# Kernel tuning notes

Hardware: AMD Instinct MI355X
Metric: run time of the kernel (lower is better)

## Reference

```python
import jax, jax.numpy as jnp
import numpy as np

DIM = 128
BATCH = 1024


def _init_linear(key, fan_in, fan_out):
    kw, kb = jax.random.split(key)
    bound = 1.0 / np.sqrt(fan_in)
    W = jax.random.uniform(kw, (fan_in, fan_out), jnp.float32, -bound, bound)
    b = jax.random.uniform(kb, (fan_out,), jnp.float32, -bound, bound)
    return W, b


def setup_inputs() -> dict:
    key = jax.random.key(0)
    kx, ky, k1, k2, k3, k4 = jax.random.split(key, 6)
    x = jax.random.normal(kx, (BATCH, DIM), jnp.float32)
    y = jax.random.normal(ky, (BATCH, DIM), jnp.float32)
    W1, b1 = _init_linear(k1, 2 * DIM, 128)
    W2, b2 = _init_linear(k2, 128, 64)
    W3, b3 = _init_linear(k3, 64, 8)
    W4, b4 = _init_linear(k4, 8, 1)
    return {"x": x, "y": y, "W1": W1, "b1": b1, "W2": W2, "b2": b2,
            "W3": W3, "b3": b3, "W4": W4, "b4": b4}


def reference(x, y, W1, b1, W2, b2, W3, b3, W4, b4):
    # Original: pairs[i, j] = concat(x[j], y[i]); scores -> [B, B]; return transpose,
    # i.e. out[a, b] = f(concat(x[a], y[b])).
    # Split first linear algebraically: concat(x, y) @ W1 = x @ W1[:d] + y @ W1[d:].
    d = x.shape[1]
    xa = x @ W1[:d]          # [B, 128]
    yb = y @ W1[d:]          # [B, 128]
    h = jax.nn.relu(xa[:, None, :] + yb[None, :, :] + b1)  # [B, B, 128]
    h = jax.nn.relu(h @ W2 + b2)                            # [B, B, 64]
    h = jax.nn.relu(h @ W3 + b3)                            # [B, B, 8]
    out = (h @ W4 + b4)[..., 0]                             # [B, B]
    return out
```

## Files before the change

kernel.cpp:

```cpp
#include <hip/hip_runtime.h>
#include <hip/hip_bf16.h>

typedef float f32x4 __attribute__((ext_vector_type(4)));
typedef float f32x16 __attribute__((ext_vector_type(16)));
typedef short s16x8 __attribute__((ext_vector_type(8)));
typedef unsigned int u32x4 __attribute__((ext_vector_type(4)));

#define YB_PITCH 132

__device__ __forceinline__ short f2bf(float v) {
    __hip_bfloat16 h = __float2bfloat16(v);
    return __builtin_bit_cast(short, h);
}
__device__ __forceinline__ unsigned cvtpk(float lo, float hi) {
    unsigned r;
    asm("v_cvt_pk_bf16_f32 %0, %1, %2" : "=v"(r) : "v"(lo), "v"(hi));
    return r;
}
__device__ __forceinline__ void swap32(unsigned &x, unsigned &y) {
    asm("v_permlane32_swap_b32 %0, %1" : "+v"(x), "+v"(y));
}

__global__ __launch_bounds__(128) void precompute_kernel(
    const float* __restrict__ x, const float* __restrict__ y,
    const float* __restrict__ W1, const float* __restrict__ b1,
    float* __restrict__ xa, float* __restrict__ yb)
{
    __shared__ float rows[8][128];
    const int bid = blockIdx.x;
    const int k = threadIdx.x;
    const bool is_x = bid < 128;
    const int r0 = (is_x ? bid : bid - 128) * 8;
    const float* src = (is_x ? x : y) + (size_t)r0 * 128;
    const float* w = is_x ? W1 : (W1 + 128 * 128);
#pragma unroll
    for (int r = 0; r < 8; ++r) rows[r][k] = src[r * 128 + k];
    __syncthreads();
    float acc[8];
    const float bias = is_x ? b1[k] : 0.0f;
#pragma unroll
    for (int r = 0; r < 8; ++r) acc[r] = bias;
    for (int d = 0; d < 128; ++d) {
        float wv = w[d * 128 + k];
#pragma unroll
        for (int r = 0; r < 8; ++r) acc[r] = fmaf(rows[r][d], wv, acc[r]);
    }
    float* dst = (is_x ? xa : yb) + (size_t)r0 * 128 + k;
#pragma unroll
    for (int r = 0; r < 8; ++r) dst[r * 128] = acc[r];
}

__global__ __launch_bounds__(256, 2) void fused_kernel(
    const float* __restrict__ xa, const float* __restrict__ yb,
    const float* __restrict__ W2, const float* __restrict__ b2,
    const float* __restrict__ W3, const float* __restrict__ b3,
    const float* __restrict__ W4, const float* __restrict__ b4,
    float* __restrict__ out)
{
    __shared__ float yb_lds[128 * YB_PITCH];
    __shared__ float xa_lds[16 * 128];

    const int tid = threadIdx.x;
    const int bid = blockIdx.x;
    const int a_chunk = bid >> 3;
    const int bquad = bid & 7;
    const int wave = tid >> 6;
    const int lane = tid & 63;
    const int half = lane >> 5;
    const int m = lane & 31;

    {
        const f32x4* ysrc = (const f32x4*)(yb + (size_t)bquad * 128 * 128);
        for (int i = tid; i < 128 * 32; i += 256) {
            int row = i >> 5, c4 = i & 31;
            *(f32x4*)&yb_lds[row * YB_PITCH + c4 * 4] = ysrc[i];
        }
        const f32x4* xsrc = (const f32x4*)(xa + (size_t)a_chunk * 16 * 128);
        for (int i = tid; i < 16 * 32; i += 256) {
            int row = i >> 5, c4 = i & 31;
            *(f32x4*)&xa_lds[row * 128 + c4 * 4] = xsrc[i];
        }
    }

    s16x8 W2a[2][8];
#pragma unroll
    for (int mt = 0; mt < 2; ++mt)
#pragma unroll
        for (int s = 0; s < 8; ++s)
#pragma unroll
            for (int j = 0; j < 8; ++j)
                W2a[mt][s][j] = f2bf(W2[(s * 16 + half * 8 + j) * 64 + mt * 32 + m]);

    s16x8 W3a[4];
#pragma unroll
    for (int s = 0; s < 4; ++s)
#pragma unroll
        for (int j = 0; j < 8; ++j)
            W3a[s][j] = (m < 8) ? f2bf(W3[(s * 16 + half * 8 + j) * 8 + m]) : (short)0;

    f32x16 b2v0, b2v1;
#pragma unroll
    for (int r = 0; r < 16; ++r) {
        int f = (r & 3) + 8 * (r >> 2) + 4 * half;
        b2v0[r] = b2[f];
        b2v1[r] = b2[f + 32];
    }
    float b3v[4], w4v[4];
#pragma unroll
    for (int j = 0; j < 4; ++j) {
        b3v[j] = b3[j + 4 * half];
        w4v[j] = W4[j + 4 * half];
    }
    const float b4s = b4[0];

    __syncthreads();

    const float* ybrow = &yb_lds[(wave * 32 + m) * YB_PITCH + half * 8];
    const int bg = bquad * 4 + wave;

    for (int ai = 0; ai < 16; ++ai) {
        const float* xr = &xa_lds[ai * 128 + half * 8];
        f32x16 c20 = b2v0, c21 = b2v1;
#pragma unroll
        for (int s = 0; s < 8; ++s) {
            f32x4 x0 = *(const f32x4*)&xr[s * 16];
            f32x4 x1 = *(const f32x4*)&xr[s * 16 + 4];
            f32x4 y0 = *(const f32x4*)&ybrow[s * 16];
            f32x4 y1 = *(const f32x4*)&ybrow[s * 16 + 4];
            f32x4 h0 = x0 + y0, h1 = x1 + y1;
            u32x4 q;
            q.x = cvtpk(fmaxf(h0.x, 0.f), fmaxf(h0.y, 0.f));
            q.y = cvtpk(fmaxf(h0.z, 0.f), fmaxf(h0.w, 0.f));
            q.z = cvtpk(fmaxf(h1.x, 0.f), fmaxf(h1.y, 0.f));
            q.w = cvtpk(fmaxf(h1.z, 0.f), fmaxf(h1.w, 0.f));
            s16x8 bfrag = __builtin_bit_cast(s16x8, q);
            c20 = __builtin_amdgcn_mfma_f32_32x32x16_bf16(W2a[0][s], bfrag, c20, 0, 0, 0);
            c21 = __builtin_amdgcn_mfma_f32_32x32x16_bf16(W2a[1][s], bfrag, c21, 0, 0, 0);
        }

        unsigned P[8], Q[8];
#pragma unroll
        for (int i = 0; i < 8; ++i) {
            P[i] = cvtpk(fmaxf(c20[2 * i], 0.f), fmaxf(c20[2 * i + 1], 0.f));
            Q[i] = cvtpk(fmaxf(c21[2 * i], 0.f), fmaxf(c21[2 * i + 1], 0.f));
        }
        s16x8 bf3[4];
        {
            unsigned w0 = P[0], w2 = P[2]; swap32(w0, w2);
            unsigned w1 = P[1], w3 = P[3]; swap32(w1, w3);
            u32x4 t; t.x = w0; t.y = w1; t.z = w2; t.w = w3;
            bf3[0] = __builtin_bit_cast(s16x8, t);
            unsigned v0 = P[4], v2 = P[6]; swap32(v0, v2);
            unsigned v1 = P[5], v3 = P[7]; swap32(v1, v3);
            u32x4 u; u.x = v0; u.y = v1; u.z = v2; u.w = v3;
            bf3[1] = __builtin_bit_cast(s16x8, u);
            unsigned a0 = Q[0], a2 = Q[2]; swap32(a0, a2);
            unsigned a1 = Q[1], a3 = Q[3]; swap32(a1, a3);
            u32x4 t2; t2.x = a0; t2.y = a1; t2.z = a2; t2.w = a3;
            bf3[2] = __builtin_bit_cast(s16x8, t2);
            unsigned e0 = Q[4], e2 = Q[6]; swap32(e0, e2);
            unsigned e1 = Q[5], e3 = Q[7]; swap32(e1, e3);
            u32x4 u2; u2.x = e0; u2.y = e1; u2.z = e2; u2.w = e3;
            bf3[3] = __builtin_bit_cast(s16x8, u2);
        }

        f32x16 c3 = {};
        c3[0] = b3v[0]; c3[1] = b3v[1]; c3[2] = b3v[2]; c3[3] = b3v[3];
#pragma unroll
        for (int s = 0; s < 4; ++s)
            c3 = __builtin_amdgcn_mfma_f32_32x32x16_bf16(W3a[s], bf3[s], c3, 0, 0, 0);

        float p = fmaxf(c3[0], 0.f) * w4v[0] + fmaxf(c3[1], 0.f) * w4v[1]
                + fmaxf(c3[2], 0.f) * w4v[2] + fmaxf(c3[3], 0.f) * w4v[3];
        unsigned pu = __builtin_bit_cast(unsigned, p);
        unsigned pv = pu;
        asm("" : "+v"(pv));
        swap32(pu, pv);
        float r = __builtin_bit_cast(float, pu) + __builtin_bit_cast(float, pv) + b4s;
        if (half == 0)
            out[(size_t)(a_chunk * 16 + ai) * 1024 + bg * 32 + m] = r;
    }
}

extern "C" void kernel_launch(void* const* d_in, const int* in_sizes, int n_in,
                              void* d_out, int out_size, void* d_ws, size_t ws_size,
                              hipStream_t stream) {
    const float* x  = (const float*)d_in[0];
    const float* y  = (const float*)d_in[1];
    const float* W1 = (const float*)d_in[2];
    const float* b1 = (const float*)d_in[3];
    const float* W2 = (const float*)d_in[4];
    const float* b2 = (const float*)d_in[5];
    const float* W3 = (const float*)d_in[6];
    const float* b3 = (const float*)d_in[7];
    const float* W4 = (const float*)d_in[8];
    const float* b4 = (const float*)d_in[9];
    float* out = (float*)d_out;

    float* xa = (float*)d_ws;
    float* yb = xa + 1024 * 128;

    precompute_kernel<<<dim3(256), dim3(128), 0, stream>>>(x, y, W1, b1, xa, yb);
    fused_kernel<<<dim3(512), dim3(256), 0, stream>>>(xa, yb, W2, b2, W3, b3, W4, b4, out);
}
```

Measured before the change: 44.36 us.

## Form the layer-1 broadcast add with an MFMA and keep yb in registers

Drops the large yb LDS tile and instead holds each wave's yb rows in registers as MFMA accumulators. For each x row it computes xa+yb with an MFMA against a ones-vector B fragment, with xa as the A operand and Y as the C input. The result is then relu'd, packed to bf16 and lane-swapped into the B-fragment layout for the layer-2 MFMA. This removes the per-iteration LDS reads of yb and the vector adds, and frees a lot of LDS for occupancy. In exchange it adds extra MFMAs, permlane swaps and register pressure, and xa is now rounded to bf16 before the add, which changes accuracy.

```diff
diff --git a/kernel.cpp b/kernel.cpp
--- a/kernel.cpp
+++ b/kernel.cpp
@@ -5,8 +5,6 @@
 typedef float f32x16 __attribute__((ext_vector_type(16)));
 typedef short s16x8 __attribute__((ext_vector_type(8)));
 typedef unsigned int u32x4 __attribute__((ext_vector_type(4)));
-
-#define YB_PITCH 132
 
 __device__ __forceinline__ short f2bf(float v) {
     __hip_bfloat16 h = __float2bfloat16(v);
@@ -57,29 +55,35 @@
     const float* __restrict__ W4, const float* __restrict__ b4,
     float* __restrict__ out)
 {
-    __shared__ float yb_lds[128 * YB_PITCH];
     __shared__ float xa_lds[16 * 128];
 
     const int tid = threadIdx.x;
     const int bid = blockIdx.x;
     const int a_chunk = bid >> 3;
-    const int bquad = bid & 7;
+    const int bq = bid & 7;
     const int wave = tid >> 6;
     const int lane = tid & 63;
     const int half = lane >> 5;
     const int m = lane & 31;
+    const int bg = bq * 4 + wave;
 
     {
-        const f32x4* ysrc = (const f32x4*)(yb + (size_t)bquad * 128 * 128);
-        for (int i = tid; i < 128 * 32; i += 256) {
-            int row = i >> 5, c4 = i & 31;
-            *(f32x4*)&yb_lds[row * YB_PITCH + c4 * 4] = ysrc[i];
-        }
         const f32x4* xsrc = (const f32x4*)(xa + (size_t)a_chunk * 16 * 128);
-        for (int i = tid; i < 16 * 32; i += 256) {
-            int row = i >> 5, c4 = i & 31;
-            *(f32x4*)&xa_lds[row * 128 + c4 * 4] = xsrc[i];
-        }
+        f32x4* dst = (f32x4*)xa_lds;
+        for (int i = tid; i < 16 * 32; i += 256) dst[i] = xsrc[i];
+    }
+
+    f32x16 Y[4];
+    {
+        const float* yrow = yb + (size_t)(bg * 32 + m) * 128 + half * 4;
+#pragma unroll
+        for (int t = 0; t < 4; ++t)
+#pragma unroll
+            for (int g = 0; g < 4; ++g) {
+                f32x4 v = *(const f32x4*)&yrow[t * 32 + g * 8];
+                Y[t][4 * g + 0] = v.x; Y[t][4 * g + 1] = v.y;
+                Y[t][4 * g + 2] = v.z; Y[t][4 * g + 3] = v.w;
+            }
     }
 
     s16x8 W2a[2][8];
@@ -97,6 +101,10 @@
 #pragma unroll
         for (int j = 0; j < 8; ++j)
             W3a[s][j] = (m < 8) ? f2bf(W3[(s * 16 + half * 8 + j) * 8 + m]) : (short)0;
+
+    u32x4 ow = {0u, 0u, 0u, 0u};
+    ow.x = (half == 0) ? 0x00003F80u : 0u;
+    const s16x8 ones = __builtin_bit_cast(s16x8, ow);
 
     f32x16 b2v0, b2v1;
 #pragma unroll
@@ -115,27 +123,37 @@
 
     __syncthreads();
 
-    const float* ybrow = &yb_lds[(wave * 32 + m) * YB_PITCH + half * 8];
-    const int bg = bquad * 4 + wave;
+    float* outp = out + (size_t)(a_chunk * 16) * 1024 + bg * 32 + m;
 
     for (int ai = 0; ai < 16; ++ai) {
-        const float* xr = &xa_lds[ai * 128 + half * 8];
         f32x16 c20 = b2v0, c21 = b2v1;
-#pragma unroll
-        for (int s = 0; s < 8; ++s) {
-            f32x4 x0 = *(const f32x4*)&xr[s * 16];
-            f32x4 x1 = *(const f32x4*)&xr[s * 16 + 4];
-            f32x4 y0 = *(const f32x4*)&ybrow[s * 16];
-            f32x4 y1 = *(const f32x4*)&ybrow[s * 16 + 4];
-            f32x4 h0 = x0 + y0, h1 = x1 + y1;
-            u32x4 q;
-            q.x = cvtpk(fmaxf(h0.x, 0.f), fmaxf(h0.y, 0.f));
-            q.y = cvtpk(fmaxf(h0.z, 0.f), fmaxf(h0.w, 0.f));
-            q.z = cvtpk(fmaxf(h1.x, 0.f), fmaxf(h1.y, 0.f));
-            q.w = cvtpk(fmaxf(h1.z, 0.f), fmaxf(h1.w, 0.f));
-            s16x8 bfrag = __builtin_bit_cast(s16x8, q);
-            c20 = __builtin_amdgcn_mfma_f32_32x32x16_bf16(W2a[0][s], bfrag, c20, 0, 0, 0);
-            c21 = __builtin_amdgcn_mfma_f32_32x32x16_bf16(W2a[1][s], bfrag, c21, 0, 0, 0);
+
+#pragma unroll
+        for (int t = 0; t < 4; ++t) {
+            float xv = xa_lds[ai * 128 + t * 32 + m];
+            unsigned pk = cvtpk(xv, xv);
+            u32x4 aw; aw.x = pk; aw.y = pk; aw.z = pk; aw.w = pk;
+            s16x8 af = __builtin_bit_cast(s16x8, aw);
+            f32x16 S = __builtin_amdgcn_mfma_f32_32x32x16_bf16(af, ones, Y[t], 0, 0, 0);
+
+            unsigned P[8];
+#pragma unroll
+            for (int i = 0; i < 8; ++i)
+                P[i] = cvtpk(fmaxf(S[2 * i], 0.f), fmaxf(S[2 * i + 1], 0.f));
+
+            unsigned w0 = P[0], w2 = P[2]; swap32(w0, w2);
+            unsigned w1 = P[1], w3 = P[3]; swap32(w1, w3);
+            u32x4 q0; q0.x = w0; q0.y = w1; q0.z = w2; q0.w = w3;
+            s16x8 bf0 = __builtin_bit_cast(s16x8, q0);
+            unsigned v0 = P[4], v2 = P[6]; swap32(v0, v2);
+            unsigned v1 = P[5], v3 = P[7]; swap32(v1, v3);
+            u32x4 q1; q1.x = v0; q1.y = v1; q1.z = v2; q1.w = v3;
+            s16x8 bf1 = __builtin_bit_cast(s16x8, q1);
+
+            c20 = __builtin_amdgcn_mfma_f32_32x32x16_bf16(W2a[0][2 * t], bf0, c20, 0, 0, 0);
+            c21 = __builtin_amdgcn_mfma_f32_32x32x16_bf16(W2a[1][2 * t], bf0, c21, 0, 0, 0);
+            c20 = __builtin_amdgcn_mfma_f32_32x32x16_bf16(W2a[0][2 * t + 1], bf1, c20, 0, 0, 0);
+            c21 = __builtin_amdgcn_mfma_f32_32x32x16_bf16(W2a[1][2 * t + 1], bf1, c21, 0, 0, 0);
         }
 
         unsigned P[8], Q[8];
@@ -178,7 +196,7 @@
         swap32(pu, pv);
         float r = __builtin_bit_cast(float, pu) + __builtin_bit_cast(float, pv) + b4s;
         if (half == 0)
-            out[(size_t)(a_chunk * 16 + ai) * 1024 + bg * 32 + m] = r;
+            outp[(size_t)ai * 1024] = r;
     }
 }
 
```

New measurement: 51.10 us. 1.15x slower.
